# Optimization experiments

Hardware: AMD Instinct MI355X
Metric: run time of the kernel (lower is better)

## Reference

```python
import jax, jax.numpy as jnp
import numpy as np

H = 16  # hidden size


def _gru_dir(x_tbi, Wih, Whh, bih, bhh, reverse):
    """Single-direction GRU over time. x_tbi: [T,B,I]. Returns [T,B,H] outputs
    aligned to original time positions (lax.scan reverse matches torch's
    bidirectional alignment). PyTorch gate order: r, z, n."""
    B = x_tbi.shape[1]
    h0 = jnp.zeros((B, Whh.shape[1]), x_tbi.dtype)
    # Precompute all input projections in one big GEMM: [T,B,3H]
    gi_all = jnp.einsum('tbi,gi->tbg', x_tbi, Wih) + bih

    def step(h, gi):
        gh = h @ Whh.T + bhh                     # [B,3H]
        i_r, i_z, i_n = jnp.split(gi, 3, axis=-1)
        h_r, h_z, h_n = jnp.split(gh, 3, axis=-1)
        r = jax.nn.sigmoid(i_r + h_r)
        z = jax.nn.sigmoid(i_z + h_z)
        n = jnp.tanh(i_n + r * h_n)
        h_new = (1.0 - z) * n + z * h
        return h_new, h_new

    _, ys = jax.lax.scan(step, h0, gi_all, reverse=reverse)
    return ys  # [T,B,H]


def _bigru_layer(x_tbi, pf, pb):
    yf = _gru_dir(x_tbi, pf[0], pf[1], pf[2], pf[3], False)
    yb = _gru_dir(x_tbi, pb[0], pb[1], pb[2], pb[3], True)
    return jnp.concatenate([yf, yb], axis=-1)  # [T,B,2H]


def setup_inputs() -> dict:
    key = jax.random.key(0)
    ks = jax.random.split(key, 20)
    B, T, I = 4096, 512, 1
    bound = 1.0 / np.sqrt(H)  # torch default init U(-1/sqrt(H), 1/sqrt(H))

    def u(k, shape):
        return jax.random.uniform(k, shape, jnp.float32, -bound, bound)

    inp = {'x': jax.random.normal(ks[0], (B, T, I), jnp.float32)}
    # layer 0: input dim 1; layer 1: input dim 2H=32. Suffix f=forward, b=backward.
    dims = {0: I, 1: 2 * H}
    i = 1
    for l in (0, 1):
        for d in ('f', 'b'):
            inp[f'W_ih_l{l}_{d}'] = u(ks[i], (3 * H, dims[l])); i += 1
            inp[f'W_hh_l{l}_{d}'] = u(ks[i], (3 * H, H)); i += 1
            inp[f'b_ih_l{l}_{d}'] = u(ks[i], (3 * H,)); i += 1
            inp[f'b_hh_l{l}_{d}'] = u(ks[i], (3 * H,)); i += 1
    return inp


def reference(x,
              W_ih_l0_f, W_hh_l0_f, b_ih_l0_f, b_hh_l0_f,
              W_ih_l0_b, W_hh_l0_b, b_ih_l0_b, b_hh_l0_b,
              W_ih_l1_f, W_hh_l1_f, b_ih_l1_f, b_hh_l1_f,
              W_ih_l1_b, W_hh_l1_b, b_ih_l1_b, b_hh_l1_b):
    x_tbi = jnp.transpose(x.astype(jnp.float32), (1, 0, 2))  # [T,B,1]
    y0 = _bigru_layer(x_tbi,
                      (W_ih_l0_f, W_hh_l0_f, b_ih_l0_f, b_hh_l0_f),
                      (W_ih_l0_b, W_hh_l0_b, b_ih_l0_b, b_hh_l0_b))
    y1 = _bigru_layer(y0,
                      (W_ih_l1_f, W_hh_l1_f, b_ih_l1_f, b_hh_l1_f),
                      (W_ih_l1_b, W_hh_l1_b, b_ih_l1_b, b_hh_l1_b))
    # out[:, -1, :] in batch_first layout == last time step of [T,B,2H]
    return y1[-1]  # [B, 2H]
```

## Files before the change

kernel.cpp:

```cpp
#include <hip/hip_runtime.h>
#include <hip/hip_fp16.h>

typedef _Float16 v2h __attribute__((ext_vector_type(2)));
typedef _Float16 h4t __attribute__((ext_vector_type(4)));
typedef _Float16 h8t __attribute__((ext_vector_type(8)));
typedef float f4t __attribute__((ext_vector_type(4)));

static constexpr int T = 512;
static constexpr int B = 4096;

static constexpr float SG = -1.4426950408889634f;
static constexpr float SN = -2.8853900817779268f;

__device__ __forceinline__ float frcp_(float x) { return __builtin_amdgcn_rcpf(x); }
__device__ __forceinline__ float exp2_(float x) {
#if __has_builtin(__builtin_amdgcn_exp2f)
    return __builtin_amdgcn_exp2f(x);
#else
    return __expf(x * 0.69314718055994531f);
#endif
}
__device__ __forceinline__ float sigp_(float p) { return frcp_(1.0f + exp2_(p)); }
__device__ __forceinline__ float tanhp_(float p) { return fmaf(2.0f, frcp_(1.0f + exp2_(p)), -1.0f); }

#define WAVE_SYNC() do { asm volatile("" ::: "memory"); \
                         __builtin_amdgcn_wave_barrier(); \
                         asm volatile("" ::: "memory"); } while (0)

__device__ __forceinline__ v2h as_h2_(unsigned u) {
    union { unsigned u; v2h h; } c; c.u = u; return c.h;
}

__device__ __forceinline__ h4t pack4_(float a, float b, float c, float d) {
    auto p0 = __builtin_amdgcn_cvt_pkrtz(a, b);
    auto p1 = __builtin_amdgcn_cvt_pkrtz(c, d);
    union { struct { decltype(p0) a, b; } p; h4t h; } cv;
    cv.p.a = p0; cv.p.b = p1;
    return cv.h;
}

__global__ void __launch_bounds__(256, 2) k_l0(
    const float* __restrict__ x,
    const float* __restrict__ Wf, const float* __restrict__ Uf,
    const float* __restrict__ bif, const float* __restrict__ bhf,
    const float* __restrict__ Wb, const float* __restrict__ Ub,
    const float* __restrict__ bib, const float* __restrict__ bhb,
    __half* __restrict__ y0f,
    __half* __restrict__ y0b)
{
    __shared__ __half hbuf[256];
    const int tid  = threadIdx.x;
    const int j    = tid & 15;
    const int dir  = (tid >> 4) & 1;
    const int s    = tid >> 5;
    const int unit = tid >> 4;
    const int b    = blockIdx.x * 8 + s;
    __half* hb = hbuf + unit * 16;

    const float* Wih = dir ? Wb : Wf;
    const float* Whh = dir ? Ub : Uf;
    const float* bih = dir ? bib : bif;
    const float* bhh = dir ? bhb : bhf;

    v2h wr[8], wz[8], wn[8];
#pragma unroll
    for (int q = 0; q < 8; ++q) {
        wr[q] = (v2h){ (_Float16)(SG * Whh[j * 16 + 2 * q]),
                       (_Float16)(SG * Whh[j * 16 + 2 * q + 1]) };
        wz[q] = (v2h){ (_Float16)(SG * Whh[(16 + j) * 16 + 2 * q]),
                       (_Float16)(SG * Whh[(16 + j) * 16 + 2 * q + 1]) };
        wn[q] = (v2h){ (_Float16)(SN * Whh[(32 + j) * 16 + 2 * q]),
                       (_Float16)(SN * Whh[(32 + j) * 16 + 2 * q + 1]) };
    }
    const float wxr  = SG * Wih[j], wxz = SG * Wih[16 + j], wxn = SN * Wih[32 + j];
    const float br   = SG * (bih[j] + bhh[j]);
    const float bz   = SG * (bih[16 + j] + bhh[16 + j]);
    const float bin_ = SN * bih[32 + j];
    const float bhn  = SN * bhh[32 + j];

    const int t0   = dir ? (T - 1) : 0;
    const int step = dir ? -1 : 1;
    const float* xp = x + (size_t)b * T + t0;
    __half* yp = (dir ? y0b : y0f) + ((size_t)t0 * B + b) * 16 + j;
    const ptrdiff_t ystep = (ptrdiff_t)step * B * 16;

    hb[j] = __half(0.0f);
    WAVE_SYNC();

    float xv = xp[0];
    float x1 = xp[step];
    const float* xq = xp + 2 * step;
    float hj = 0.0f;

    for (int it = 0; it < T; ++it) {
        float x2 = *xq;
        if (it < T - 3) xq += step;
        const uint4* hp = reinterpret_cast<const uint4*>(hb);
        uint4 u0 = hp[0], u1 = hp[1];
        float ar = fmaf(xv, wxr, br);
        float az = fmaf(xv, wxz, bz);
        float hn = bhn;
        {
            v2h hh;
            hh = as_h2_(u0.x);
            ar = __builtin_amdgcn_fdot2(hh, wr[0], ar, false);
            az = __builtin_amdgcn_fdot2(hh, wz[0], az, false);
            hn = __builtin_amdgcn_fdot2(hh, wn[0], hn, false);
            hh = as_h2_(u0.y);
            ar = __builtin_amdgcn_fdot2(hh, wr[1], ar, false);
            az = __builtin_amdgcn_fdot2(hh, wz[1], az, false);
            hn = __builtin_amdgcn_fdot2(hh, wn[1], hn, false);
            hh = as_h2_(u0.z);
            ar = __builtin_amdgcn_fdot2(hh, wr[2], ar, false);
            az = __builtin_amdgcn_fdot2(hh, wz[2], az, false);
            hn = __builtin_amdgcn_fdot2(hh, wn[2], hn, false);
            hh = as_h2_(u0.w);
            ar = __builtin_amdgcn_fdot2(hh, wr[3], ar, false);
            az = __builtin_amdgcn_fdot2(hh, wz[3], az, false);
            hn = __builtin_amdgcn_fdot2(hh, wn[3], hn, false);
            hh = as_h2_(u1.x);
            ar = __builtin_amdgcn_fdot2(hh, wr[4], ar, false);
            az = __builtin_amdgcn_fdot2(hh, wz[4], az, false);
            hn = __builtin_amdgcn_fdot2(hh, wn[4], hn, false);
            hh = as_h2_(u1.y);
            ar = __builtin_amdgcn_fdot2(hh, wr[5], ar, false);
            az = __builtin_amdgcn_fdot2(hh, wz[5], az, false);
            hn = __builtin_amdgcn_fdot2(hh, wn[5], hn, false);
            hh = as_h2_(u1.z);
            ar = __builtin_amdgcn_fdot2(hh, wr[6], ar, false);
            az = __builtin_amdgcn_fdot2(hh, wz[6], az, false);
            hn = __builtin_amdgcn_fdot2(hh, wn[6], hn, false);
            hh = as_h2_(u1.w);
            ar = __builtin_amdgcn_fdot2(hh, wr[7], ar, false);
            az = __builtin_amdgcn_fdot2(hh, wz[7], az, false);
            hn = __builtin_amdgcn_fdot2(hh, wn[7], hn, false);
        }
        float r = sigp_(ar), z = sigp_(az);
        float n = tanhp_(fmaf(r, hn, fmaf(xv, wxn, bin_)));
        hj = fmaf(z, hj - n, n);
        __half hf = __float2half(hj);
        *yp = hf;
        yp += ystep;
        WAVE_SYNC();
        hb[j] = hf;
        WAVE_SYNC();
        xv = x1; x1 = x2;
    }
}

__global__ void __launch_bounds__(64, 1) k_l1m(
    const __half* __restrict__ y0f, const __half* __restrict__ y0b,
    const float* __restrict__ Wih1, const float* __restrict__ Whh1,
    const float* __restrict__ bih1, const float* __restrict__ bhh1,
    const float* __restrict__ Wih1b,
    const float* __restrict__ bih1b, const float* __restrict__ bhh1b,
    float* __restrict__ out)
{
    const int lane = threadIdx.x & 63;
    const int c = lane & 15;
    const int g = lane >> 4;
    const int b = blockIdx.x * 16 + c;

    h8t Air, Aiz, Ain;
    {
        const float* pr = Wih1 + (size_t)c * 32 + 8 * g;
        const float* pz = Wih1 + (size_t)(16 + c) * 32 + 8 * g;
        const float* pn = Wih1 + (size_t)(32 + c) * 32 + 8 * g;
#pragma unroll
        for (int e = 0; e < 8; ++e) {
            Air[e] = (_Float16)(SG * pr[e]);
            Aiz[e] = (_Float16)(SG * pz[e]);
            Ain[e] = (_Float16)(SN * pn[e]);
        }
    }
    h4t Ahr, Ahz, Ahn;
    {
        const float* pr = Whh1 + (size_t)c * 16 + 4 * g;
        const float* pz = Whh1 + (size_t)(16 + c) * 16 + 4 * g;
        const float* pn = Whh1 + (size_t)(32 + c) * 16 + 4 * g;
#pragma unroll
        for (int e = 0; e < 4; ++e) {
            Ahr[e] = (_Float16)(SG * pr[e]);
            Ahz[e] = (_Float16)(SG * pz[e]);
            Ahn[e] = (_Float16)(SN * pn[e]);
        }
    }
    f4t Crb, Czb, Cnb, Chn;
#pragma unroll
    for (int i = 0; i < 4; ++i) {
        const int row = 4 * g + i;
        Crb[i] = SG * (bih1[row] + bhh1[row]);
        Czb[i] = SG * (bih1[16 + row] + bhh1[16 + row]);
        Cnb[i] = SN * bih1[32 + row];
        Chn[i] = SN * bhh1[32 + row];
    }

    const __half* ysrc = (g < 2) ? y0f : y0b;
    const uint4* yp = reinterpret_cast<const uint4*>(
        ysrc + (size_t)b * 16 + (size_t)(g & 1) * 8);
    const size_t ystr = (size_t)B * 2;

    uint4 buf[8];
#pragma unroll
    for (int i = 0; i < 8; ++i) buf[i] = yp[(size_t)i * ystr];

    float h[4] = {0.0f, 0.0f, 0.0f, 0.0f};
    h4t Bh = {};

#pragma unroll 8
    for (int it = 0; it < T; ++it) {
        uint4 ya = buf[it & 7];
        const size_t tn = (it + 8 < T) ? (size_t)(it + 8) : (size_t)(T - 1);
        buf[it & 7] = yp[tn * ystr];
        h8t By;
        { union { uint4 u; h8t h; } cv; cv.u = ya; By = cv.h; }
        f4t Dr = __builtin_amdgcn_mfma_f32_16x16x32_f16(Air, By, Crb, 0, 0, 0);
        f4t Dz = __builtin_amdgcn_mfma_f32_16x16x32_f16(Aiz, By, Czb, 0, 0, 0);
        f4t Dn = __builtin_amdgcn_mfma_f32_16x16x32_f16(Ain, By, Cnb, 0, 0, 0);
        f4t Er = __builtin_amdgcn_mfma_f32_16x16x16f16(Ahr, Bh, Dr, 0, 0, 0);
        f4t Ez = __builtin_amdgcn_mfma_f32_16x16x16f16(Ahz, Bh, Dz, 0, 0, 0);
        f4t En = __builtin_amdgcn_mfma_f32_16x16x16f16(Ahn, Bh, Chn, 0, 0, 0);
#pragma unroll
        for (int i = 0; i < 4; ++i) {
            float r = sigp_(Er[i]);
            float z = sigp_(Ez[i]);
            float n = tanhp_(fmaf(r, En[i], Dn[i]));
            h[i] = fmaf(z, h[i] - n, n);
        }
        Bh = pack4_(h[0], h[1], h[2], h[3]);
    }

#pragma unroll
    for (int i = 0; i < 4; ++i)
        out[(size_t)b * 32 + 4 * g + i] = h[i];

    uint4 yfin = buf[(T - 1) & 7];
    h8t Abr, Abz, Abn;
    {
        const float* pr = Wih1b + (size_t)c * 32 + 8 * g;
        const float* pz = Wih1b + (size_t)(16 + c) * 32 + 8 * g;
        const float* pn = Wih1b + (size_t)(32 + c) * 32 + 8 * g;
#pragma unroll
        for (int e = 0; e < 8; ++e) {
            Abr[e] = (_Float16)(SG * pr[e]);
            Abz[e] = (_Float16)(SG * pz[e]);
            Abn[e] = (_Float16)(SN * pn[e]);
        }
    }
    f4t Cbr, Cbz, Cbn;
    float ghn[4];
#pragma unroll
    for (int i = 0; i < 4; ++i) {
        const int row = 4 * g + i;
        Cbr[i] = SG * (bih1b[row] + bhh1b[row]);
        Cbz[i] = SG * (bih1b[16 + row] + bhh1b[16 + row]);
        Cbn[i] = SN * bih1b[32 + row];
        ghn[i] = SN * bhh1b[32 + row];
    }
    h8t By;
    { union { uint4 u; h8t h; } cv; cv.u = yfin; By = cv.h; }
    f4t Dr = __builtin_amdgcn_mfma_f32_16x16x32_f16(Abr, By, Cbr, 0, 0, 0);
    f4t Dz = __builtin_amdgcn_mfma_f32_16x16x32_f16(Abz, By, Cbz, 0, 0, 0);
    f4t Dn = __builtin_amdgcn_mfma_f32_16x16x32_f16(Abn, By, Cbn, 0, 0, 0);
#pragma unroll
    for (int i = 0; i < 4; ++i) {
        float r = sigp_(Dr[i]);
        float z = sigp_(Dz[i]);
        float n = tanhp_(fmaf(r, ghn[i], Dn[i]));
        out[(size_t)b * 32 + 16 + 4 * g + i] = (1.0f - z) * n;
    }
}

extern "C" void kernel_launch(void* const* d_in, const int* in_sizes, int n_in,
                              void* d_out, int out_size, void* d_ws, size_t ws_size,
                              hipStream_t stream) {
    const float* x     = (const float*)d_in[0];
    const float* Wih0f = (const float*)d_in[1];
    const float* Whh0f = (const float*)d_in[2];
    const float* bih0f = (const float*)d_in[3];
    const float* bhh0f = (const float*)d_in[4];
    const float* Wih0b = (const float*)d_in[5];
    const float* Whh0b = (const float*)d_in[6];
    const float* bih0b = (const float*)d_in[7];
    const float* bhh0b = (const float*)d_in[8];
    const float* Wih1f = (const float*)d_in[9];
    const float* Whh1f = (const float*)d_in[10];
    const float* bih1f = (const float*)d_in[11];
    const float* bhh1f = (const float*)d_in[12];
    const float* Wih1b = (const float*)d_in[13];
    const float* bih1b = (const float*)d_in[15];
    const float* bhh1b = (const float*)d_in[16];

    __half* y0f = (__half*)d_ws;
    __half* y0b = y0f + (size_t)T * B * 16;
    float* out = (float*)d_out;

    hipLaunchKernelGGL(k_l0, dim3(B * 2 / 16), dim3(256), 0, stream,
                       x, Wih0f, Whh0f, bih0f, bhh0f,
                       Wih0b, Whh0b, bih0b, bhh0b, y0f, y0b);
    hipLaunchKernelGGL(k_l1m, dim3(B / 16), dim3(64), 0, stream,
                       y0f, y0b, Wih1f, Whh1f, bih1f, bhh1f,
                       Wih1b, bih1b, bhh1b, out);
}
```

Before: 250.4 us.

## Interleave forward and backward GRU chains per thread and share reciprocals

The layer-0 kernel now has each thread run both the forward and backward recurrence for one hidden unit. That gives two independent dependency chains per thread for ILP, and the grid is halved to B/16 blocks with launch bounds of one block per SM. Both kernels also merge the sigmoid and tanh reciprocals, computing one rcp of a product and recovering each value with multiplies, so fewer transcendental ops sit on the serial critical path. Costs are more registers per thread, fewer waves for latency hiding, and a small accuracy change because the product of the denominators can overflow for large exponents.

```diff
diff --git a/kernel.cpp b/kernel.cpp
--- a/kernel.cpp
+++ b/kernel.cpp
@@ -39,112 +39,114 @@
     return cv.h;
 }
 
-__global__ void __launch_bounds__(256, 2) k_l0(
+__global__ void __launch_bounds__(256, 1) k_l0p(
     const float* __restrict__ x,
     const float* __restrict__ Wf, const float* __restrict__ Uf,
     const float* __restrict__ bif, const float* __restrict__ bhf,
     const float* __restrict__ Wb, const float* __restrict__ Ub,
     const float* __restrict__ bib, const float* __restrict__ bhb,
-    __half* __restrict__ y0f,
-    __half* __restrict__ y0b)
+    __half* __restrict__ y0f, __half* __restrict__ y0b)
 {
-    __shared__ __half hbuf[256];
-    const int tid  = threadIdx.x;
-    const int j    = tid & 15;
-    const int dir  = (tid >> 4) & 1;
-    const int s    = tid >> 5;
-    const int unit = tid >> 4;
-    const int b    = blockIdx.x * 8 + s;
-    __half* hb = hbuf + unit * 16;
-
-    const float* Wih = dir ? Wb : Wf;
-    const float* Whh = dir ? Ub : Uf;
-    const float* bih = dir ? bib : bif;
-    const float* bhh = dir ? bhb : bhf;
-
-    v2h wr[8], wz[8], wn[8];
+    __shared__ __half hbuf[512];
+    const int tid = threadIdx.x;
+    const int j   = tid & 15;
+    const int grp = tid >> 4;
+    const int b   = blockIdx.x * 16 + grp;
+    __half* hbA = hbuf + grp * 16;
+    __half* hbB = hbuf + 256 + grp * 16;
+
+    v2h wrA[8], wzA[8], wnA[8], wrB[8], wzB[8], wnB[8];
 #pragma unroll
     for (int q = 0; q < 8; ++q) {
-        wr[q] = (v2h){ (_Float16)(SG * Whh[j * 16 + 2 * q]),
-                       (_Float16)(SG * Whh[j * 16 + 2 * q + 1]) };
-        wz[q] = (v2h){ (_Float16)(SG * Whh[(16 + j) * 16 + 2 * q]),
-                       (_Float16)(SG * Whh[(16 + j) * 16 + 2 * q + 1]) };
-        wn[q] = (v2h){ (_Float16)(SN * Whh[(32 + j) * 16 + 2 * q]),
-                       (_Float16)(SN * Whh[(32 + j) * 16 + 2 * q + 1]) };
-    }
-    const float wxr  = SG * Wih[j], wxz = SG * Wih[16 + j], wxn = SN * Wih[32 + j];
-    const float br   = SG * (bih[j] + bhh[j]);
-    const float bz   = SG * (bih[16 + j] + bhh[16 + j]);
-    const float bin_ = SN * bih[32 + j];
-    const float bhn  = SN * bhh[32 + j];
-
-    const int t0   = dir ? (T - 1) : 0;
-    const int step = dir ? -1 : 1;
-    const float* xp = x + (size_t)b * T + t0;
-    __half* yp = (dir ? y0b : y0f) + ((size_t)t0 * B + b) * 16 + j;
-    const ptrdiff_t ystep = (ptrdiff_t)step * B * 16;
-
-    hb[j] = __half(0.0f);
+        wrA[q] = (v2h){ (_Float16)(SG * Uf[j * 16 + 2 * q]),
+                        (_Float16)(SG * Uf[j * 16 + 2 * q + 1]) };
+        wzA[q] = (v2h){ (_Float16)(SG * Uf[(16 + j) * 16 + 2 * q]),
+                        (_Float16)(SG * Uf[(16 + j) * 16 + 2 * q + 1]) };
+        wnA[q] = (v2h){ (_Float16)(SN * Uf[(32 + j) * 16 + 2 * q]),
+                        (_Float16)(SN * Uf[(32 + j) * 16 + 2 * q + 1]) };
+        wrB[q] = (v2h){ (_Float16)(SG * Ub[j * 16 + 2 * q]),
+                        (_Float16)(SG * Ub[j * 16 + 2 * q + 1]) };
+        wzB[q] = (v2h){ (_Float16)(SG * Ub[(16 + j) * 16 + 2 * q]),
+                        (_Float16)(SG * Ub[(16 + j) * 16 + 2 * q + 1]) };
+        wnB[q] = (v2h){ (_Float16)(SN * Ub[(32 + j) * 16 + 2 * q]),
+                        (_Float16)(SN * Ub[(32 + j) * 16 + 2 * q + 1]) };
+    }
+    const float wxrA = SG * Wf[j], wxzA = SG * Wf[16 + j], wxnA = SN * Wf[32 + j];
+    const float brA  = SG * (bif[j] + bhf[j]);
+    const float bzA  = SG * (bif[16 + j] + bhf[16 + j]);
+    const float binA = SN * bif[32 + j];
+    const float bhnA = SN * bhf[32 + j];
+    const float wxrB = SG * Wb[j], wxzB = SG * Wb[16 + j], wxnB = SN * Wb[32 + j];
+    const float brB  = SG * (bib[j] + bhb[j]);
+    const float bzB  = SG * (bib[16 + j] + bhb[16 + j]);
+    const float binB = SN * bib[32 + j];
+    const float bhnB = SN * bhb[32 + j];
+
+    const float* xrow = x + (size_t)b * T;
+    __half* ypA = y0f + (size_t)b * 16 + j;
+    __half* ypB = y0b + ((size_t)(T - 1) * B + b) * 16 + j;
+    const ptrdiff_t ystp = (ptrdiff_t)B * 16;
+
+    hbA[j] = __half(0.0f);
+    hbB[j] = __half(0.0f);
     WAVE_SYNC();
 
-    float xv = xp[0];
-    float x1 = xp[step];
-    const float* xq = xp + 2 * step;
-    float hj = 0.0f;
+    float xvA = xrow[0],      x1A = xrow[1];
+    float xvB = xrow[T - 1],  x1B = xrow[T - 2];
+    const float* xqA = xrow + 2;
+    const float* xqB = xrow + T - 3;
+    float hA = 0.0f, hB = 0.0f;
 
     for (int it = 0; it < T; ++it) {
-        float x2 = *xq;
-        if (it < T - 3) xq += step;
-        const uint4* hp = reinterpret_cast<const uint4*>(hb);
-        uint4 u0 = hp[0], u1 = hp[1];
-        float ar = fmaf(xv, wxr, br);
-        float az = fmaf(xv, wxz, bz);
-        float hn = bhn;
-        {
-            v2h hh;
-            hh = as_h2_(u0.x);
-            ar = __builtin_amdgcn_fdot2(hh, wr[0], ar, false);
-            az = __builtin_amdgcn_fdot2(hh, wz[0], az, false);
-            hn = __builtin_amdgcn_fdot2(hh, wn[0], hn, false);
-            hh = as_h2_(u0.y);
-            ar = __builtin_amdgcn_fdot2(hh, wr[1], ar, false);
-            az = __builtin_amdgcn_fdot2(hh, wz[1], az, false);
-            hn = __builtin_amdgcn_fdot2(hh, wn[1], hn, false);
-            hh = as_h2_(u0.z);
-            ar = __builtin_amdgcn_fdot2(hh, wr[2], ar, false);
-            az = __builtin_amdgcn_fdot2(hh, wz[2], az, false);
-            hn = __builtin_amdgcn_fdot2(hh, wn[2], hn, false);
-            hh = as_h2_(u0.w);
-            ar = __builtin_amdgcn_fdot2(hh, wr[3], ar, false);
-            az = __builtin_amdgcn_fdot2(hh, wz[3], az, false);
-            hn = __builtin_amdgcn_fdot2(hh, wn[3], hn, false);
-            hh = as_h2_(u1.x);
-            ar = __builtin_amdgcn_fdot2(hh, wr[4], ar, false);
-            az = __builtin_amdgcn_fdot2(hh, wz[4], az, false);
-            hn = __builtin_amdgcn_fdot2(hh, wn[4], hn, false);
-            hh = as_h2_(u1.y);
-            ar = __builtin_amdgcn_fdot2(hh, wr[5], ar, false);
-            az = __builtin_amdgcn_fdot2(hh, wz[5], az, false);
-            hn = __builtin_amdgcn_fdot2(hh, wn[5], hn, false);
-            hh = as_h2_(u1.z);
-            ar = __builtin_amdgcn_fdot2(hh, wr[6], ar, false);
-            az = __builtin_amdgcn_fdot2(hh, wz[6], az, false);
-            hn = __builtin_amdgcn_fdot2(hh, wn[6], hn, false);
-            hh = as_h2_(u1.w);
-            ar = __builtin_amdgcn_fdot2(hh, wr[7], ar, false);
-            az = __builtin_amdgcn_fdot2(hh, wz[7], az, false);
-            hn = __builtin_amdgcn_fdot2(hh, wn[7], hn, false);
-        }
-        float r = sigp_(ar), z = sigp_(az);
-        float n = tanhp_(fmaf(r, hn, fmaf(xv, wxn, bin_)));
-        hj = fmaf(z, hj - n, n);
-        __half hf = __float2half(hj);
-        *yp = hf;
-        yp += ystep;
+        float x2A = *xqA, x2B = *xqB;
+        if (it < T - 3) { xqA += 1; xqB -= 1; }
+        const uint4* hpA = reinterpret_cast<const uint4*>(hbA);
+        const uint4* hpB = reinterpret_cast<const uint4*>(hbB);
+        uint4 a0 = hpA[0], a1 = hpA[1];
+        uint4 b0 = hpB[0], b1 = hpB[1];
+
+        float arA = fmaf(xvA, wxrA, brA), azA = fmaf(xvA, wxzA, bzA), hnA = bhnA;
+        float arB = fmaf(xvB, wxrB, brB), azB = fmaf(xvB, wxzB, bzB), hnB = bhnB;
+        const unsigned ha[8] = { a0.x, a0.y, a0.z, a0.w, a1.x, a1.y, a1.z, a1.w };
+        const unsigned hbw[8] = { b0.x, b0.y, b0.z, b0.w, b1.x, b1.y, b1.z, b1.w };
+#pragma unroll
+        for (int q = 0; q < 8; ++q) {
+            v2h hh = as_h2_(ha[q]);
+            arA = __builtin_amdgcn_fdot2(hh, wrA[q], arA, false);
+            azA = __builtin_amdgcn_fdot2(hh, wzA[q], azA, false);
+            hnA = __builtin_amdgcn_fdot2(hh, wnA[q], hnA, false);
+            v2h gg = as_h2_(hbw[q]);
+            arB = __builtin_amdgcn_fdot2(gg, wrB[q], arB, false);
+            azB = __builtin_amdgcn_fdot2(gg, wzB[q], azB, false);
+            hnB = __builtin_amdgcn_fdot2(gg, wnB[q], hnB, false);
+        }
+        float EaA = exp2_(arA), EzA = exp2_(azA);
+        float EaB = exp2_(arB), EzB = exp2_(azB);
+        float aA = 1.0f + EaA, bA = 1.0f + EzA;
+        float aB = 1.0f + EaB, bB = 1.0f + EzB;
+        float invA = frcp_(aA * bA);
+        float invB = frcp_(aB * bB);
+        float rA = invA * bA, zA = invA * aA;
+        float rB = invB * bB, zB = invB * aB;
+        float pnA = fmaf(rA, hnA, fmaf(xvA, wxnA, binA));
+        float pnB = fmaf(rB, hnB, fmaf(xvB, wxnB, binB));
+        float cA = 1.0f + exp2_(pnA);
+        float cB = 1.0f + exp2_(pnB);
+        float invn = frcp_(cA * cB);
+        float nA = fmaf(2.0f * cB, invn, -1.0f);
+        float nB = fmaf(2.0f * cA, invn, -1.0f);
+        hA = fmaf(zA, hA - nA, nA);
+        hB = fmaf(zB, hB - nB, nB);
+        __half hfA = __float2half(hA);
+        __half hfB = __float2half(hB);
+        *ypA = hfA; ypA += ystp;
+        *ypB = hfB; ypB -= ystp;
         WAVE_SYNC();
-        hb[j] = hf;
+        hbA[j] = hfA;
+        hbB[j] = hfB;
         WAVE_SYNC();
-        xv = x1; x1 = x2;
+        xvA = x1A; x1A = x2A;
+        xvB = x1B; x1B = x2B;
     }
 }
 
@@ -220,13 +222,28 @@
         f4t Er = __builtin_amdgcn_mfma_f32_16x16x16f16(Ahr, Bh, Dr, 0, 0, 0);
         f4t Ez = __builtin_amdgcn_mfma_f32_16x16x16f16(Ahz, Bh, Dz, 0, 0, 0);
         f4t En = __builtin_amdgcn_mfma_f32_16x16x16f16(Ahn, Bh, Chn, 0, 0, 0);
+        float zv[4], cc[4];
 #pragma unroll
         for (int i = 0; i < 4; ++i) {
-            float r = sigp_(Er[i]);
-            float z = sigp_(Ez[i]);
-            float n = tanhp_(fmaf(r, En[i], Dn[i]));
-            h[i] = fmaf(z, h[i] - n, n);
-        }
+            float Ea = exp2_(Er[i]);
+            float Ezv = exp2_(Ez[i]);
+            float a = 1.0f + Ea, bb2 = 1.0f + Ezv;
+            float inv = frcp_(a * bb2);
+            float r = inv * bb2;
+            zv[i] = inv * a;
+            float pn = fmaf(r, En[i], Dn[i]);
+            cc[i] = 1.0f + exp2_(pn);
+        }
+        float inv01 = frcp_(cc[0] * cc[1]);
+        float inv23 = frcp_(cc[2] * cc[3]);
+        float n0 = fmaf(2.0f * cc[1], inv01, -1.0f);
+        float n1 = fmaf(2.0f * cc[0], inv01, -1.0f);
+        float n2 = fmaf(2.0f * cc[3], inv23, -1.0f);
+        float n3 = fmaf(2.0f * cc[2], inv23, -1.0f);
+        h[0] = fmaf(zv[0], h[0] - n0, n0);
+        h[1] = fmaf(zv[1], h[1] - n1, n1);
+        h[2] = fmaf(zv[2], h[2] - n2, n2);
+        h[3] = fmaf(zv[3], h[3] - n3, n3);
         Bh = pack4_(h[0], h[1], h[2], h[3]);
     }
 
@@ -295,7 +312,7 @@
     __half* y0b = y0f + (size_t)T * B * 16;
     float* out = (float*)d_out;
 
-    hipLaunchKernelGGL(k_l0, dim3(B * 2 / 16), dim3(256), 0, stream,
+    hipLaunchKernelGGL(k_l0p, dim3(B / 16), dim3(256), 0, stream,
                        x, Wih0f, Whh0f, bih0f, bhh0f,
                        Wih0b, Whh0b, bih0b, bhh0b, y0f, y0b);
     hipLaunchKernelGGL(k_l1m, dim3(B / 16), dim3(64), 0, stream,
```

Result: slower. 306.0 us (+22.2%).
